# Kernel optimization log

Hardware: AMD Instinct MI355X
Metric: run time of the kernel (lower is better)

The kernel has to match this reference:

```python
import jax, jax.numpy as jnp
import numpy as np

B, S, D, H = 2, 2048, 1024, 16
DK = D // H
EPS = 1e-5


def setup_inputs() -> dict:
    key = jax.random.key(0)
    ks = jax.random.split(key, 6)
    std = (2.0 / (D + D)) ** 0.5
    return {
        "x": jax.random.normal(ks[0], (B, S, D), dtype=jnp.float32),
        "W_Q": jax.random.normal(ks[1], (D, D), dtype=jnp.float32) * std,
        "W_K": jax.random.normal(ks[2], (D, D), dtype=jnp.float32) * std,
        "W_V": jax.random.normal(ks[3], (D, D), dtype=jnp.float32) * std,
        "W_O": jax.random.normal(ks[4], (D, D), dtype=jnp.float32) * std,
        "gain": jnp.ones((D,), dtype=jnp.float32),
        "positions": jnp.arange(S, dtype=jnp.int64 if jax.config.jax_enable_x64 else jnp.int32),
        "theta": 10000,
        "max_seq_len": 2048,
    }


def rmsnorm(x, gain):
    xf = x.astype(jnp.float32)
    rms = jnp.sqrt(jnp.mean(xf * xf, axis=-1, keepdims=True) + EPS)
    return ((xf / rms) * gain).astype(x.dtype)


def apply_rope(x, sin, cos):
    # x: [..., seq, dk]; sin/cos: [seq, dk//2] broadcast over leading dims
    x_even = x[..., 0::2]
    x_odd = x[..., 1::2]
    r_even = x_even * cos - x_odd * sin
    r_odd = x_odd * cos + x_even * sin
    return jnp.stack([r_even, r_odd], axis=-1).reshape(x.shape)


def reference(x, W_Q, W_K, W_V, W_O, gain, positions, theta, max_seq_len):
    seq_len = x.shape[-2]
    Q = jnp.einsum('od,bsd->bso', W_Q, x)
    K = jnp.einsum('od,bsd->bso', W_K, x)
    V = jnp.einsum('od,bsd->bso', W_V, x)
    # RMSNorm over full d_model BEFORE head split (as in original)
    Q = rmsnorm(Q, gain)
    K = rmsnorm(K, gain)
    # split heads: [b, h, s, dk]
    Q = Q.reshape(*Q.shape[:-1], H, DK).swapaxes(-3, -2)
    K = K.reshape(*K.shape[:-1], H, DK).swapaxes(-3, -2)
    V = V.reshape(*V.shape[:-1], H, DK).swapaxes(-3, -2)
    # RoPE tables
    exponents = 2.0 * jnp.arange(DK // 2, dtype=jnp.float32) / DK
    inv_freq = 1.0 / (jnp.float32(theta) ** exponents)
    angles = positions.astype(jnp.float32)[:, None] * inv_freq[None, :]  # [S, DK//2]
    sin, cos = jnp.sin(angles), jnp.cos(angles)
    Q = apply_rope(Q, sin, cos)
    K = apply_rope(K, sin, cos)
    # causal attention
    scores = jnp.einsum('bhqd,bhkd->bhqk', Q, K) / jnp.sqrt(jnp.float32(DK))
    causal = jnp.tril(jnp.ones((seq_len, seq_len), dtype=bool))
    scores = jnp.where(causal, scores, -jnp.inf)
    attn = jax.nn.softmax(scores, axis=-1)
    out = jnp.einsum('bhqk,bhkd->bhqd', attn, V)
    out = out.swapaxes(-3, -2).reshape(*x.shape[:-1], D)
    return jnp.einsum('of,bsf->bso', W_O, out)
```

## Files before the change

### kernel.cpp

```cpp
#include <hip/hip_runtime.h>
#include <hip/hip_bf16.h>

typedef __attribute__((ext_vector_type(8))) __bf16 bf16x8;
typedef __attribute__((ext_vector_type(4))) __bf16 bf16x4;
typedef __attribute__((ext_vector_type(4))) float  f32x4;

#define S_LEN 2048
#define D_DIM 1024
#define NH    16
#define GK    1024
#define GN    1024

__device__ __forceinline__ float fast_exp2(float x) {
#if __has_builtin(__builtin_amdgcn_exp2f)
  return __builtin_amdgcn_exp2f(x);
#else
  return exp2f(x);
#endif
}

__device__ __forceinline__ void gld_lds16(const void* g, void* l) {
  __builtin_amdgcn_global_load_lds(
      (const __attribute__((address_space(1))) unsigned int*)g,
      (__attribute__((address_space(3))) unsigned int*)l, 16, 0, 0);
}

__global__ __launch_bounds__(256) void cast_all(
    const float* __restrict__ x,  const float* __restrict__ wq, const float* __restrict__ wk,
    const float* __restrict__ wv, const float* __restrict__ wo,
    __bf16* __restrict__ xb, __bf16* __restrict__ wqb, __bf16* __restrict__ wkb,
    __bf16* __restrict__ wvb, __bf16* __restrict__ wob)
{
  const int NTOT = 2 << 20;
  for (int i = blockIdx.x * 256 + threadIdx.x; i < NTOT; i += 1024 * 256) {
    const float* s; __bf16* d; int off;
    if (i < (1 << 20)) { s = x; d = xb; off = i; }
    else {
      const int j = i - (1 << 20);
      const int r = j >> 18; off = j & ((1 << 18) - 1);
      s = (r == 0) ? wq : (r == 1) ? wk : (r == 2) ? wv : wo;
      d = (r == 0) ? wqb : (r == 1) ? wkb : (r == 2) ? wvb : wob;
    }
    float4 v = ((const float4*)s)[off];
    bf16x4 o = { (__bf16)v.x, (__bf16)v.y, (__bf16)v.z, (__bf16)v.w };
    ((bf16x4*)d)[off] = o;
  }
}

__global__ __launch_bounds__(256, 6) void gemm_qkv(
    const __bf16* __restrict__ A,
    const __bf16* __restrict__ W0, const __bf16* __restrict__ W1, const __bf16* __restrict__ W2,
    __bf16* __restrict__ C0, __bf16* __restrict__ C1, __bf16* __restrict__ VtOut)
{
  const int bid = blockIdx.x;
  const int e = bid & 7, mg = e >> 1, ng = e & 1;
  const int q = bid >> 3;
  const int mode = q % 3;
  const int t = q / 3;
  const int m0 = (mg * 16 + (t & 15)) * 64;
  const int n0 = (ng * 4 + (t >> 4)) * 128;
  const __bf16* Wm = (mode == 0) ? W0 : (mode == 1) ? W1 : W2;

  __shared__ __align__(16) __bf16 As[64 * 64];
  __shared__ __align__(16) __bf16 Bs[128 * 64];

  const int tid  = threadIdx.x;
  const int lane = tid & 63;
  const int w    = tid >> 6;
  const int wr   = w >> 1, wc = w & 1;
  const int lm   = lane & 15, qd = lane >> 4;

  const __bf16* ap[2]; int loA[2];
  #pragma unroll
  for (int j = 0; j < 2; j++) {
    const int c = tid + 256 * j;
    const int r = c >> 3, cpos = c & 7;
    ap[j] = A + (size_t)(m0 + r) * GK + (cpos ^ (r & 7)) * 8;
    loA[j] = c * 8;
  }
  const __bf16* bp[4]; int loB[4];
  #pragma unroll
  for (int j = 0; j < 4; j++) {
    const int c = tid + 256 * j;
    const int r = c >> 3, cpos = c & 7;
    bp[j] = Wm + (size_t)(n0 + r) * GK + (cpos ^ (r & 7)) * 8;
    loB[j] = c * 8;
  }

  const int sw = lm & 7;

  f32x4 zero = {0.f, 0.f, 0.f, 0.f};
  f32x4 acc[2][4];
  #pragma unroll
  for (int i = 0; i < 2; i++)
    #pragma unroll
    for (int j = 0; j < 4; j++) acc[i][j] = zero;

  for (int k0 = 0; k0 < GK; k0 += 64) {
    #pragma unroll
    for (int j = 0; j < 2; j++) gld_lds16(ap[j] + k0, &As[loA[j]]);
    #pragma unroll
    for (int j = 0; j < 4; j++) gld_lds16(bp[j] + k0, &Bs[loB[j]]);
    __syncthreads();
    #pragma unroll
    for (int half = 0; half < 2; half++) {
      const int cph = ((qd + 4 * half) ^ sw) * 8;
      bf16x8 af[2], bfv[4];
      #pragma unroll
      for (int i = 0; i < 2; i++) af[i]  = *(const bf16x8*)&As[(wr * 32 + i * 16 + lm) * 64 + cph];
      #pragma unroll
      for (int j = 0; j < 4; j++) bfv[j] = *(const bf16x8*)&Bs[(wc * 64 + j * 16 + lm) * 64 + cph];
      #pragma unroll
      for (int i = 0; i < 2; i++)
        #pragma unroll
        for (int j = 0; j < 4; j++)
          acc[i][j] = __builtin_amdgcn_mfma_f32_16x16x32_bf16(af[i], bfv[j], acc[i][j], 0, 0, 0);
    }
    __syncthreads();
  }

  if (mode < 2) {
    __bf16* C = (mode == 0) ? C0 : C1;
    #pragma unroll
    for (int i = 0; i < 2; i++) {
      const int row = m0 + wr * 32 + i * 16 + qd * 4;
      #pragma unroll
      for (int j = 0; j < 4; j++) {
        const int col = n0 + wc * 64 + j * 16 + lm;
        #pragma unroll
        for (int r = 0; r < 4; r++)
          C[(size_t)(row + r) * GN + col] = (__bf16)acc[i][j][r];
      }
    }
  } else {
    #pragma unroll
    for (int i = 0; i < 2; i++) {
      const int row = m0 + wr * 32 + i * 16 + qd * 4;
      const int b = row >> 11, s = row & (S_LEN - 1);
      #pragma unroll
      for (int j = 0; j < 4; j++) {
        const int col = n0 + wc * 64 + j * 16 + lm;
        const int h = col >> 6, d = col & 63;
        bf16x4 o = { (__bf16)acc[i][j][0], (__bf16)acc[i][j][1],
                     (__bf16)acc[i][j][2], (__bf16)acc[i][j][3] };
        *(bf16x4*)(VtOut + (((size_t)(b * NH + h) * 64 + d) * S_LEN + s)) = o;
      }
    }
  }
}

__global__ __launch_bounds__(256, 6) void gemm_out64(
    const __bf16* __restrict__ A, const __bf16* __restrict__ Wm, float* __restrict__ C)
{
  const int bid = blockIdx.x;
  const int e = bid & 7, mg = e >> 1, ng = e & 1;
  const int q = bid >> 3;
  const int m0 = (mg * 16 + (q & 15)) * 64;
  const int n0 = (ng * 4 + (q >> 4)) * 128;

  __shared__ __align__(16) __bf16 As[64 * 64];
  __shared__ __align__(16) __bf16 Bs[128 * 64];

  const int tid  = threadIdx.x;
  const int lane = tid & 63;
  const int w    = tid >> 6;
  const int wr   = w >> 1, wc = w & 1;
  const int lm   = lane & 15, qd = lane >> 4;

  const __bf16* ap[2]; int loA[2];
  #pragma unroll
  for (int j = 0; j < 2; j++) {
    const int c = tid + 256 * j;
    const int r = c >> 3, cpos = c & 7;
    ap[j] = A + (size_t)(m0 + r) * GK + (cpos ^ (r & 7)) * 8;
    loA[j] = c * 8;
  }
  const __bf16* bp[4]; int loB[4];
  #pragma unroll
  for (int j = 0; j < 4; j++) {
    const int c = tid + 256 * j;
    const int r = c >> 3, cpos = c & 7;
    bp[j] = Wm + (size_t)(n0 + r) * GK + (cpos ^ (r & 7)) * 8;
    loB[j] = c * 8;
  }

  const int sw = lm & 7;

  f32x4 zero = {0.f, 0.f, 0.f, 0.f};
  f32x4 acc[2][4];
  #pragma unroll
  for (int i = 0; i < 2; i++)
    #pragma unroll
    for (int j = 0; j < 4; j++) acc[i][j] = zero;

  for (int k0 = 0; k0 < GK; k0 += 64) {
    #pragma unroll
    for (int j = 0; j < 2; j++) gld_lds16(ap[j] + k0, &As[loA[j]]);
    #pragma unroll
    for (int j = 0; j < 4; j++) gld_lds16(bp[j] + k0, &Bs[loB[j]]);
    __syncthreads();
    #pragma unroll
    for (int half = 0; half < 2; half++) {
      const int cph = ((qd + 4 * half) ^ sw) * 8;
      bf16x8 af[2], bfv[4];
      #pragma unroll
      for (int i = 0; i < 2; i++) af[i]  = *(const bf16x8*)&As[(wr * 32 + i * 16 + lm) * 64 + cph];
      #pragma unroll
      for (int j = 0; j < 4; j++) bfv[j] = *(const bf16x8*)&Bs[(wc * 64 + j * 16 + lm) * 64 + cph];
      #pragma unroll
      for (int i = 0; i < 2; i++)
        #pragma unroll
        for (int j = 0; j < 4; j++)
          acc[i][j] = __builtin_amdgcn_mfma_f32_16x16x32_bf16(af[i], bfv[j], acc[i][j], 0, 0, 0);
    }
    __syncthreads();
  }

  #pragma unroll
  for (int i = 0; i < 2; i++) {
    const int row = m0 + wr * 32 + i * 16 + qd * 4;
    #pragma unroll
    for (int j = 0; j < 4; j++) {
      const int col = n0 + wc * 64 + j * 16 + lm;
      #pragma unroll
      for (int r = 0; r < 4; r++)
        C[(size_t)(row + r) * GN + col] = acc[i][j][r];
    }
  }
}

__global__ __launch_bounds__(256) void norm_rope(
    const __bf16* __restrict__ Qf, const __bf16* __restrict__ Kf,
    const float* __restrict__ gain, const int* __restrict__ positions,
    const int* __restrict__ theta_p,
    __bf16* __restrict__ Qh, __bf16* __restrict__ Kh)
{
  const int row = blockIdx.x;
  const int s = row & (S_LEN - 1), b = row >> 11;
  const int t = threadIdx.x, d0 = t * 4;

  const bf16x4 qv = *(const bf16x4*)(Qf + (size_t)row * D_DIM + d0);
  const bf16x4 kv = *(const bf16x4*)(Kf + (size_t)row * D_DIM + d0);
  const float q0 = (float)qv[0], q1 = (float)qv[1], q2 = (float)qv[2], q3 = (float)qv[3];
  const float k0 = (float)kv[0], k1 = (float)kv[1], k2 = (float)kv[2], k3 = (float)kv[3];

  float sq = q0 * q0 + q1 * q1 + q2 * q2 + q3 * q3;
  float sk = k0 * k0 + k1 * k1 + k2 * k2 + k3 * k3;
  #pragma unroll
  for (int off = 32; off; off >>= 1) { sq += __shfl_xor(sq, off); sk += __shfl_xor(sk, off); }
  __shared__ float red[8];
  const int lane = t & 63, wv = t >> 6;
  if (lane == 0) { red[wv] = sq; red[4 + wv] = sk; }
  __syncthreads();
  sq = red[0] + red[1] + red[2] + red[3];
  sk = red[4] + red[5] + red[6] + red[7];
  const float invq = rsqrtf(sq * (1.0f / 1024.0f) + 1e-5f);
  const float invk = rsqrtf(sk * (1.0f / 1024.0f) + 1e-5f);

  const float4 g = *(const float4*)(gain + d0);
  const float qn0 = q0 * invq * g.x, qn1 = q1 * invq * g.y;
  const float qn2 = q2 * invq * g.z, qn3 = q3 * invq * g.w;
  const float kn0 = k0 * invk * g.x, kn1 = k1 * invk * g.y;
  const float kn2 = k2 * invk * g.z, kn3 = k3 * invk * g.w;

  const float pos = (float)positions[s];
  const float th  = (float)theta_p[0];
  const int idx = d0 & 63, h = d0 >> 6, p0 = idx >> 1;
  const float lg32 = __log2f(th) * (1.0f / 32.0f);
  const float f0 = fast_exp2(-(float)p0 * lg32);
  const float f1 = fast_exp2(-(float)(p0 + 1) * lg32);
  float s0, cc0, s1, cc1;
  __sincosf(pos * f0, &s0, &cc0);
  __sincosf(pos * f1, &s1, &cc1);

  const float qe0 = qn0 * cc0 - qn1 * s0, qo0 = qn1 * cc0 + qn0 * s0;
  const float qe1 = qn2 * cc1 - qn3 * s1, qo1 = qn3 * cc1 + qn2 * s1;
  const float ke0 = kn0 * cc0 - kn1 * s0, ko0 = kn1 * cc0 + kn0 * s0;
  const float ke1 = kn2 * cc1 - kn3 * s1, ko1 = kn3 * cc1 + kn2 * s1;

  const size_t obase = ((size_t)((b * NH + h) * S_LEN + s)) * 64 + idx;
  bf16x4 qo = { (__bf16)qe0, (__bf16)qo0, (__bf16)qe1, (__bf16)qo1 };
  bf16x4 ko = { (__bf16)ke0, (__bf16)ko0, (__bf16)ke1, (__bf16)ko1 };
  *(bf16x4*)(Qh + obase) = qo;
  *(bf16x4*)(Kh + obase) = ko;
}

__global__ __launch_bounds__(256) void attn_fwd(
    const __bf16* __restrict__ Qh, const __bf16* __restrict__ Kh,
    const __bf16* __restrict__ Vt, __bf16* __restrict__ Ob)
{
  const int bid = blockIdx.x;
  const int g   = bid >> 5, gj = g & 7, gs = g >> 3;
  const int qt  = (gs == 0) ? 31 - gj : (gs == 1) ? gj : (gs == 2) ? 23 - gj : 8 + gj;
  const int rr  = bid & 31;
  const int bh  = (rr & 7) * 4 + (rr >> 3);
  const int tid = threadIdx.x, lane = tid & 63, w = tid >> 6;
  const int lm = lane & 15, qd = lane >> 4;

  __shared__ __align__(16) __bf16 smem[8192 + 8192 + 4096];
  __bf16* Ks = smem;
  __bf16* Vs = smem + 8192;
  __bf16* Pw = smem + 16384 + w * 1024;

  const int row0 = qt * 64 + w * 16;
  const size_t qbase = (size_t)bh * S_LEN * 64;
  const bf16x8 aq0 = *(const bf16x8*)(Qh + qbase + (size_t)(row0 + lm) * 64 + qd * 8);
  const bf16x8 aq1 = *(const bf16x8*)(Qh + qbase + (size_t)(row0 + lm) * 64 + 32 + qd * 8);

  const __bf16* Kb = Kh + (size_t)bh * S_LEN * 64;
  const __bf16* Vb = Vt + (size_t)bh * 64 * S_LEN;
  const int c0 = tid, c1 = 256 + tid;
  const int kr0 = c0 >> 3, kr1 = c1 >> 3;
  const int kg0 = ((c0 & 7) ^ (kr0 & 7)) * 8;
  const int kg1 = ((c1 & 7) ^ (kr1 & 7)) * 8;
  const int cpA = (qd ^ (lm & 7)) * 8;
  const int cpB = cpA ^ 32;

  auto stage = [&](int buf, int k0) {
    __bf16* Kd = Ks + buf * 4096;
    __bf16* Vd = Vs + buf * 4096;
    gld_lds16(Kb + (size_t)(k0 + kr0) * 64 + kg0, &Kd[c0 * 8]);
    gld_lds16(Kb + (size_t)(k0 + kr1) * 64 + kg1, &Kd[c1 * 8]);
    gld_lds16(Vb + (size_t)kr0 * S_LEN + k0 + kg0, &Vd[c0 * 8]);
    gld_lds16(Vb + (size_t)kr1 * S_LEN + k0 + kg1, &Vd[c1 * 8]);
  };

  const float SC2 = 0.125f * 1.44269504089f;
  const float OFF = 12.0f;
  f32x4 zero = {0.f, 0.f, 0.f, 0.f};
  float l[4] = {0.f, 0.f, 0.f, 0.f};
  f32x4 o[4];
  #pragma unroll
  for (int jb = 0; jb < 4; jb++) o[jb] = zero;

  stage(0, 0);

  const int rowg = row0 + qd * 4;
  const int pxor = qd * 4;

  for (int kt = 0; kt <= qt; ++kt) {
    const int cur = kt & 1;
    __syncthreads();
    if (kt < qt) stage(cur ^ 1, (kt + 1) * 64);

    const __bf16* Kc = Ks + cur * 4096;
    const __bf16* Vc = Vs + cur * 4096;
    const int k0 = kt * 64;

    float p[4][4];
    const bool diag = (kt == qt);
    #pragma unroll
    for (int kb = 0; kb < 4; kb++) {
      const int krow = (kb * 16 + lm) * 64;
      const bf16x8 bk0 = *(const bf16x8*)&Kc[krow + cpA];
      const bf16x8 bk1 = *(const bf16x8*)&Kc[krow + cpB];
      f32x4 sc = zero;
      sc = __builtin_amdgcn_mfma_f32_16x16x32_bf16(aq0, bk0, sc, 0, 0, 0);
      sc = __builtin_amdgcn_mfma_f32_16x16x32_bf16(aq1, bk1, sc, 0, 0, 0);
      if (diag) {
        const int colg = k0 + kb * 16 + lm;
        #pragma unroll
        for (int r = 0; r < 4; r++) {
          const float e = fast_exp2(fmaf(sc[r], SC2, -OFF));
          p[kb][r] = (colg <= rowg + r) ? e : 0.f;
          l[r] += p[kb][r];
        }
      } else {
        #pragma unroll
        for (int r = 0; r < 4; r++) {
          p[kb][r] = fast_exp2(fmaf(sc[r], SC2, -OFF));
          l[r] += p[kb][r];
        }
      }
    }

    #pragma unroll
    for (int kb = 0; kb < 4; kb++) {
      const int cb = kb * 2 + (lm >> 3), wi = lm & 7;
      #pragma unroll
      for (int r = 0; r < 4; r++) {
        const int prow = pxor + r;
        Pw[prow * 64 + ((cb ^ (prow & 7)) << 3) + wi] = (__bf16)p[kb][r];
      }
    }

    const bf16x8 ap0 = *(const bf16x8*)&Pw[lm * 64 + cpA];
    const bf16x8 ap1 = *(const bf16x8*)&Pw[lm * 64 + cpB];
    #pragma unroll
    for (int jb = 0; jb < 4; jb++) {
      const int vrow = (jb * 16 + lm) * 64;
      const bf16x8 bv0 = *(const bf16x8*)&Vc[vrow + cpA];
      const bf16x8 bv1 = *(const bf16x8*)&Vc[vrow + cpB];
      o[jb] = __builtin_amdgcn_mfma_f32_16x16x32_bf16(ap1, bv1,
              __builtin_amdgcn_mfma_f32_16x16x32_bf16(ap0, bv0, o[jb], 0, 0, 0), 0, 0, 0);
    }
  }

  const int b = bh >> 4, h = bh & 15;
  #pragma unroll
  for (int r = 0; r < 4; r++) {
    float lr = l[r];
    #pragma unroll
    for (int off = 8; off; off >>= 1) lr += __shfl_xor(lr, off);
    const float inv = 1.0f / lr;
    const size_t base = ((size_t)(b * S_LEN + rowg + r)) * D_DIM + h * 64;
    #pragma unroll
    for (int jb = 0; jb < 4; jb++)
      Ob[base + jb * 16 + lm] = (__bf16)(o[jb][r] * inv);
  }
}

extern "C" void kernel_launch(void* const* d_in, const int* in_sizes, int n_in,
                              void* d_out, int out_size, void* d_ws, size_t ws_size,
                              hipStream_t stream)
{
  (void)in_sizes; (void)n_in; (void)out_size; (void)ws_size;
  const float* x    = (const float*)d_in[0];
  const float* WQ   = (const float*)d_in[1];
  const float* WK   = (const float*)d_in[2];
  const float* WV   = (const float*)d_in[3];
  const float* WO   = (const float*)d_in[4];
  const float* gain = (const float*)d_in[5];
  const int* positions = (const int*)d_in[6];
  const int* theta     = (const int*)d_in[7];
  float* out = (float*)d_out;

  char* ws = (char*)d_ws;
  const size_t MB = 1024 * 1024;
  __bf16* xb  = (__bf16*)(ws + 0);
  __bf16* WQb = (__bf16*)(ws + 8  * MB);
  __bf16* WKb = (__bf16*)(ws + 10 * MB);
  __bf16* WVb = (__bf16*)(ws + 12 * MB);
  __bf16* WOb = (__bf16*)(ws + 14 * MB);
  __bf16* Qfb = (__bf16*)(ws + 16 * MB);
  __bf16* Kfb = (__bf16*)(ws + 24 * MB);
  __bf16* Vt  = (__bf16*)(ws + 32 * MB);
  __bf16* Qh  = (__bf16*)(ws + 40 * MB);
  __bf16* Kh  = (__bf16*)(ws + 48 * MB);
  __bf16* Ob  = (__bf16*)(ws + 56 * MB);

  cast_all<<<1024, 256, 0, stream>>>(x, WQ, WK, WV, WO, xb, WQb, WKb, WVb, WOb);
  gemm_qkv<<<1536, 256, 0, stream>>>(xb, WQb, WKb, WVb, Qfb, Kfb, Vt);
  norm_rope<<<4096, 256, 0, stream>>>(Qfb, Kfb, gain, positions, theta, Qh, Kh);
  attn_fwd<<<1024, 256, 0, stream>>>(Qh, Kh, Vt, Ob);
  gemm_out64<<<512, 256, 0, stream>>>(Ob, WOb, out);
}
```

Baseline: 178.5 us.

## Process 128 query rows per attention block to reuse staged K/V tiles

Each attention workgroup now handles two 64-row query sub-tiles (128 rows), with each wave processing one 16-row slice in each sub-tile. This lets every K/V tile staged into LDS feed twice as many QK and PV MFMAs, halving the global-to-LDS K/V traffic per query row and the block count. The q-tile scheduling is simplified to pair long and short tiles, the P scratch in LDS is doubled, and launch bounds request 3 blocks per CU. The cost is more registers per thread, fewer blocks (512) to balance causal work, and a larger per-block critical path.

```diff
diff --git a/kernel.cpp b/kernel.cpp
--- a/kernel.cpp
+++ b/kernel.cpp
@@ -285,27 +285,32 @@
   *(bf16x4*)(Kh + obase) = ko;
 }
 
-__global__ __launch_bounds__(256) void attn_fwd(
+__global__ __launch_bounds__(256, 3) void attn_fwd(
     const __bf16* __restrict__ Qh, const __bf16* __restrict__ Kh,
     const __bf16* __restrict__ Vt, __bf16* __restrict__ Ob)
 {
   const int bid = blockIdx.x;
   const int g   = bid >> 5, gj = g & 7, gs = g >> 3;
-  const int qt  = (gs == 0) ? 31 - gj : (gs == 1) ? gj : (gs == 2) ? 23 - gj : 8 + gj;
+  const int qt  = gs ? gj : 15 - gj;
   const int rr  = bid & 31;
   const int bh  = (rr & 7) * 4 + (rr >> 3);
   const int tid = threadIdx.x, lane = tid & 63, w = tid >> 6;
   const int lm = lane & 15, qd = lane >> 4;
 
-  __shared__ __align__(16) __bf16 smem[8192 + 8192 + 4096];
+  __shared__ __align__(16) __bf16 smem[8192 + 8192 + 8192];
   __bf16* Ks = smem;
   __bf16* Vs = smem + 8192;
-  __bf16* Pw = smem + 16384 + w * 1024;
-
-  const int row0 = qt * 64 + w * 16;
+  __bf16* Pw = smem + 16384 + w * 2048;
+
+  const int row0 = qt * 128 + w * 16;
   const size_t qbase = (size_t)bh * S_LEN * 64;
-  const bf16x8 aq0 = *(const bf16x8*)(Qh + qbase + (size_t)(row0 + lm) * 64 + qd * 8);
-  const bf16x8 aq1 = *(const bf16x8*)(Qh + qbase + (size_t)(row0 + lm) * 64 + 32 + qd * 8);
+  bf16x8 aq[2][2];
+  #pragma unroll
+  for (int s = 0; s < 2; s++) {
+    const size_t qoff = qbase + (size_t)(row0 + s * 64 + lm) * 64;
+    aq[s][0] = *(const bf16x8*)(Qh + qoff + qd * 8);
+    aq[s][1] = *(const bf16x8*)(Qh + qoff + 32 + qd * 8);
+  }
 
   const __bf16* Kb = Kh + (size_t)bh * S_LEN * 64;
   const __bf16* Vb = Vt + (size_t)bh * 64 * S_LEN;
@@ -328,85 +333,98 @@
   const float SC2 = 0.125f * 1.44269504089f;
   const float OFF = 12.0f;
   f32x4 zero = {0.f, 0.f, 0.f, 0.f};
-  float l[4] = {0.f, 0.f, 0.f, 0.f};
-  f32x4 o[4];
-  #pragma unroll
-  for (int jb = 0; jb < 4; jb++) o[jb] = zero;
+  float l[2][4] = {{0.f,0.f,0.f,0.f},{0.f,0.f,0.f,0.f}};
+  f32x4 o[2][4];
+  #pragma unroll
+  for (int s = 0; s < 2; s++)
+    #pragma unroll
+    for (int jb = 0; jb < 4; jb++) o[s][jb] = zero;
 
   stage(0, 0);
 
-  const int rowg = row0 + qd * 4;
+  const int ktmax = 2 * qt + 1;
   const int pxor = qd * 4;
 
-  for (int kt = 0; kt <= qt; ++kt) {
+  for (int kt = 0; kt <= ktmax; ++kt) {
     const int cur = kt & 1;
     __syncthreads();
-    if (kt < qt) stage(cur ^ 1, (kt + 1) * 64);
+    if (kt < ktmax) stage(cur ^ 1, (kt + 1) * 64);
 
     const __bf16* Kc = Ks + cur * 4096;
     const __bf16* Vc = Vs + cur * 4096;
     const int k0 = kt * 64;
 
-    float p[4][4];
-    const bool diag = (kt == qt);
-    #pragma unroll
-    for (int kb = 0; kb < 4; kb++) {
-      const int krow = (kb * 16 + lm) * 64;
-      const bf16x8 bk0 = *(const bf16x8*)&Kc[krow + cpA];
-      const bf16x8 bk1 = *(const bf16x8*)&Kc[krow + cpB];
-      f32x4 sc = zero;
-      sc = __builtin_amdgcn_mfma_f32_16x16x32_bf16(aq0, bk0, sc, 0, 0, 0);
-      sc = __builtin_amdgcn_mfma_f32_16x16x32_bf16(aq1, bk1, sc, 0, 0, 0);
-      if (diag) {
-        const int colg = k0 + kb * 16 + lm;
+    #pragma unroll
+    for (int s = 0; s < 2; s++) {
+      if (s == 0 && kt > 2 * qt) continue;
+      const int rowg = row0 + s * 64 + qd * 4;
+      const bool diag = (kt == 2 * qt + s);
+      __bf16* Ps = Pw + s * 1024;
+
+      float p[4][4];
+      #pragma unroll
+      for (int kb = 0; kb < 4; kb++) {
+        const int krow = (kb * 16 + lm) * 64;
+        const bf16x8 bk0 = *(const bf16x8*)&Kc[krow + cpA];
+        const bf16x8 bk1 = *(const bf16x8*)&Kc[krow + cpB];
+        f32x4 sc = zero;
+        sc = __builtin_amdgcn_mfma_f32_16x16x32_bf16(aq[s][0], bk0, sc, 0, 0, 0);
+        sc = __builtin_amdgcn_mfma_f32_16x16x32_bf16(aq[s][1], bk1, sc, 0, 0, 0);
+        if (diag) {
+          const int colg = k0 + kb * 16 + lm;
+          #pragma unroll
+          for (int r = 0; r < 4; r++) {
+            const float e = fast_exp2(fmaf(sc[r], SC2, -OFF));
+            p[kb][r] = (colg <= rowg + r) ? e : 0.f;
+            l[s][r] += p[kb][r];
+          }
+        } else {
+          #pragma unroll
+          for (int r = 0; r < 4; r++) {
+            p[kb][r] = fast_exp2(fmaf(sc[r], SC2, -OFF));
+            l[s][r] += p[kb][r];
+          }
+        }
+      }
+
+      #pragma unroll
+      for (int kb = 0; kb < 4; kb++) {
+        const int cb = kb * 2 + (lm >> 3), wi = lm & 7;
         #pragma unroll
         for (int r = 0; r < 4; r++) {
-          const float e = fast_exp2(fmaf(sc[r], SC2, -OFF));
-          p[kb][r] = (colg <= rowg + r) ? e : 0.f;
-          l[r] += p[kb][r];
-        }
-      } else {
-        #pragma unroll
-        for (int r = 0; r < 4; r++) {
-          p[kb][r] = fast_exp2(fmaf(sc[r], SC2, -OFF));
-          l[r] += p[kb][r];
+          const int prow = pxor + r;
+          Ps[prow * 64 + ((cb ^ (prow & 7)) << 3) + wi] = (__bf16)p[kb][r];
         }
       }
-    }
-
-    #pragma unroll
-    for (int kb = 0; kb < 4; kb++) {
-      const int cb = kb * 2 + (lm >> 3), wi = lm & 7;
-      #pragma unroll
-      for (int r = 0; r < 4; r++) {
-        const int prow = pxor + r;
-        Pw[prow * 64 + ((cb ^ (prow & 7)) << 3) + wi] = (__bf16)p[kb][r];
+
+      const bf16x8 ap0 = *(const bf16x8*)&Ps[lm * 64 + cpA];
+      const bf16x8 ap1 = *(const bf16x8*)&Ps[lm * 64 + cpB];
+      #pragma unroll
+      for (int jb = 0; jb < 4; jb++) {
+        const int vrow = (jb * 16 + lm) * 64;
+        const bf16x8 bv0 = *(const bf16x8*)&Vc[vrow + cpA];
+        const bf16x8 bv1 = *(const bf16x8*)&Vc[vrow + cpB];
+        o[s][jb] = __builtin_amdgcn_mfma_f32_16x16x32_bf16(ap1, bv1,
+                   __builtin_amdgcn_mfma_f32_16x16x32_bf16(ap0, bv0, o[s][jb], 0, 0, 0), 0, 0, 0);
       }
     }
-
-    const bf16x8 ap0 = *(const bf16x8*)&Pw[lm * 64 + cpA];
-    const bf16x8 ap1 = *(const bf16x8*)&Pw[lm * 64 + cpB];
-    #pragma unroll
-    for (int jb = 0; jb < 4; jb++) {
-      const int vrow = (jb * 16 + lm) * 64;
-      const bf16x8 bv0 = *(const bf16x8*)&Vc[vrow + cpA];
-      const bf16x8 bv1 = *(const bf16x8*)&Vc[vrow + cpB];
-      o[jb] = __builtin_amdgcn_mfma_f32_16x16x32_bf16(ap1, bv1,
-              __builtin_amdgcn_mfma_f32_16x16x32_bf16(ap0, bv0, o[jb], 0, 0, 0), 0, 0, 0);
-    }
   }
 
   const int b = bh >> 4, h = bh & 15;
   #pragma unroll
-  for (int r = 0; r < 4; r++) {
-    float lr = l[r];
-    #pragma unroll
-    for (int off = 8; off; off >>= 1) lr += __shfl_xor(lr, off);
-    const float inv = 1.0f / lr;
-    const size_t base = ((size_t)(b * S_LEN + rowg + r)) * D_DIM + h * 64;
-    #pragma unroll
-    for (int jb = 0; jb < 4; jb++)
-      Ob[base + jb * 16 + lm] = (__bf16)(o[jb][r] * inv);
+  for (int s = 0; s < 2; s++) {
+    const int rowg = row0 + s * 64 + qd * 4;
+    #pragma unroll
+    for (int r = 0; r < 4; r++) {
+      float lr = l[s][r];
+      #pragma unroll
+      for (int off = 8; off; off >>= 1) lr += __shfl_xor(lr, off);
+      const float inv = 1.0f / lr;
+      const size_t base = ((size_t)(b * S_LEN + rowg + r)) * D_DIM + h * 64;
+      #pragma unroll
+      for (int jb = 0; jb < 4; jb++)
+        Ob[base + jb * 16 + lm] = (__bf16)(o[s][jb][r] * inv);
+    }
   }
 }
 
@@ -442,6 +460,6 @@
   cast_all<<<1024, 256, 0, stream>>>(x, WQ, WK, WV, WO, xb, WQb, WKb, WVb, WOb);
   gemm_qkv<<<1536, 256, 0, stream>>>(xb, WQb, WKb, WVb, Qfb, Kfb, Vt);
   norm_rope<<<4096, 256, 0, stream>>>(Qfb, Kfb, gain, positions, theta, Qh, Kh);
-  attn_fwd<<<1024, 256, 0, stream>>>(Qh, Kh, Vt, Ob);
+  attn_fwd<<<512, 256, 0, stream>>>(Qh, Kh, Vt, Ob);
   gemm_out64<<<512, 256, 0, stream>>>(Ob, WOb, out);
 }
```

Result: slower. 194.0 us (+8.7%).
